# Kernel optimization log

Measured on AMD Instinct MI355X. Metric: run time of the kernel, lower is better.

Reference implementation:

```python
import jax, jax.numpy as jnp
import numpy as np

C = 256
D = C // 8  # query/key channels


def setup_inputs() -> dict:
    key = jax.random.key(0)
    ks = jax.random.split(key, 7)
    x = jax.random.normal(ks[0], (4, C, 64, 64), dtype=jnp.float32)
    s1 = 1.0 / np.sqrt(C)
    w1 = jax.random.normal(ks[1], (D, C), dtype=jnp.float32) * s1
    b1 = jax.random.normal(ks[2], (D,), dtype=jnp.float32) * 0.01
    w2 = jax.random.normal(ks[3], (D, C), dtype=jnp.float32) * s1
    b2 = jax.random.normal(ks[4], (D,), dtype=jnp.float32) * 0.01
    w3 = jax.random.normal(ks[5], (C, C), dtype=jnp.float32) * s1
    b3 = jax.random.normal(ks[6], (C,), dtype=jnp.float32) * 0.01
    return {"x": x, "w1": w1, "b1": b1, "w2": w2, "b2": b2, "w3": w3, "b3": b3}


def reference(x, w1, b1, w2, b2, w3, b3):
    B, Cc, W, H = x.shape
    N = W * H
    xf = x.reshape(B, Cc, N)  # [B, C, N] flattened spatial
    # 1x1 convs are per-pixel linear maps over channels
    q = jnp.einsum('dc,bcn->bnd', w1, xf) + b1  # [B, N, D]
    k = jnp.einsum('dc,bcn->bdn', w2, xf) + b2[:, None]  # [B, D, N]
    v = jnp.einsum('oc,bcn->bon', w3, xf) + b3[:, None]  # [B, C, N]
    energy = jnp.einsum('bnd,bdm->bnm', q, k)  # [B, N, N]
    attn = jax.nn.softmax(energy, axis=-1)
    out = jnp.einsum('bcm,bnm->bcn', v, attn)  # bmm(V, attn^T)
    out = out.reshape(B, Cc, W, H) + x
    return out
```

## Files before the change

kernel.cpp:

```cpp
#include <hip/hip_runtime.h>
#include <hip/hip_fp16.h>

typedef _Float16 half8 __attribute__((ext_vector_type(8)));
typedef _Float16 half2v __attribute__((ext_vector_type(2)));
typedef float f32x16 __attribute__((ext_vector_type(16)));
typedef float f32x4v __attribute__((ext_vector_type(4)));

#define MFMA16(A, B, C) __builtin_amdgcn_mfma_f32_32x32x16_f16((A), (B), (C), 0, 0, 0)

__device__ __forceinline__ f32x16 fzero16() {
  f32x16 z;
#pragma unroll
  for (int i = 0; i < 16; ++i) z[i] = 0.0f;
  return z;
}

__device__ __forceinline__ float max16(float vm, const f32x16& s) {
  const float g1 = fmaxf(fmaxf(s[0], s[1]), s[2]);
  const float g2 = fmaxf(fmaxf(s[3], s[4]), s[5]);
  const float g3 = fmaxf(fmaxf(s[6], s[7]), s[8]);
  const float g4 = fmaxf(fmaxf(s[9], s[10]), s[11]);
  const float g5 = fmaxf(fmaxf(s[12], s[13]), s[14]);
  const float h1 = fmaxf(fmaxf(g1, g2), g3);
  const float h2 = fmaxf(fmaxf(g4, g5), s[15]);
  return fmaxf(fmaxf(vm, h1), h2);
}

__global__ __launch_bounds__(256) void wprep_kernel(
    const float* __restrict__ w1, const float* __restrict__ w2,
    const float* __restrict__ w3,
    _Float16* __restrict__ w1p, _Float16* __restrict__ w2p,
    _Float16* __restrict__ w3p)
{
  const int t = threadIdx.x;
  const int blk = blockIdx.x;
  if (blk < 32) {
    const int cot = blk >> 2, sub = blk & 3;
    for (int e = sub * 2048 + t; e < sub * 2048 + 2048; e += 256) {
      const int j = e & 7, l = (e >> 3) & 63, cs = e >> 9;
      const int lr = l & 31, h = l >> 5;
      const int row = cot * 32 + lr;
      const int col = cs * 16 + 4 * h + (j & 3) + 8 * (j >> 2);
      w3p[((cot * 16 + cs) * 64 + l) * 8 + j] = (_Float16)w3[row * 256 + col];
    }
  } else {
    const int sub = blk - 32;
    for (int e = sub * 1024 + t; e < sub * 1024 + 1024; e += 256) {
      const int j = e & 7, l = (e >> 3) & 63, cs = e >> 9;
      const int lr = l & 31, h = l >> 5;
      const int col = cs * 16 + 4 * h + (j & 3) + 8 * (j >> 2);
      const int idx = (cs * 64 + l) * 8 + j;
      w1p[idx] = (_Float16)w1[lr * 256 + col];
      w2p[idx] = (_Float16)w2[lr * 256 + col];
    }
  }
}

__global__ __launch_bounds__(256) void qkv_proj_kernel(
    const float* __restrict__ x,
    const _Float16* __restrict__ w1p, const float* __restrict__ b1,
    const _Float16* __restrict__ w2p, const float* __restrict__ b2,
    const _Float16* __restrict__ w3p, const float* __restrict__ b3,
    _Float16* __restrict__ qb, _Float16* __restrict__ kb,
    _Float16* __restrict__ vb)
{
  __shared__ f32x4v red[4][2][4][64];
  const int t = threadIdx.x, w = t >> 6, l = t & 63;
  const int lr = l & 31, h = l >> 5;
  const int b = blockIdx.x >> 7;
  const int nt = blockIdx.x & 127;
  const float* xb = x + (size_t)b * 256 * 4096 + nt * 32 + lr;
  const int cot0 = w * 2, cot1 = w * 2 + 1;

  f32x16 accq = fzero16(), acck = fzero16();
  f32x16 accv0 = fzero16(), accv1 = fzero16();

  for (int cs = 0; cs < 16; ++cs) {
    const int c0 = cs * 16 + 4 * h;
    half8 xh;
#pragma unroll
    for (int j = 0; j < 8; ++j) {
      const int c = c0 + (j & 3) + 8 * (j >> 2);
      xh[j] = (_Float16)xb[(size_t)c * 4096];
    }
    const half8 wh0 = *(const half8*)&w3p[((cot0 * 16 + cs) * 64 + l) * 8];
    const half8 wh1 = *(const half8*)&w3p[((cot1 * 16 + cs) * 64 + l) * 8];
    accv0 = MFMA16(xh, wh0, accv0);
    accv1 = MFMA16(xh, wh1, accv1);
    if ((cs >> 2) == w) {
      const half8 w1h = *(const half8*)&w1p[(cs * 64 + l) * 8];
      const half8 w2h = *(const half8*)&w2p[(cs * 64 + l) * 8];
      accq = MFMA16(w1h, xh, accq);
      acck = MFMA16(w2h, xh, acck);
    }
  }

  const float bv0 = b3[cot0 * 32 + lr];
  const float bv1 = b3[cot1 * 32 + lr];
#pragma unroll
  for (int hfq = 0; hfq < 2; ++hfq) {
    half8 p0, p1;
#pragma unroll
    for (int j = 0; j < 8; ++j) {
      p0[j] = (_Float16)(accv0[8 * hfq + j] + bv0);
      p1[j] = (_Float16)(accv1[8 * hfq + j] + bv1);
    }
    const int ms = nt * 2 + hfq;
    *(half8*)&vb[((((size_t)b * 256 + ms) * 8 + cot0) * 64 + l) * 8] = p0;
    *(half8*)&vb[((((size_t)b * 256 + ms) * 8 + cot1) * 64 + l) * 8] = p1;
  }

#pragma unroll
  for (int i4 = 0; i4 < 4; ++i4) {
    f32x4v q4, k4;
#pragma unroll
    for (int c = 0; c < 4; ++c) { q4[c] = accq[4 * i4 + c]; k4[c] = acck[4 * i4 + c]; }
    red[w][0][i4][l] = q4;
    red[w][1][i4][l] = k4;
  }
  __syncthreads();
  if (w < 2) {
    _Float16* dst = (w == 0) ? qb : kb;
    const float* bias = (w == 0) ? b1 : b2;
    f32x16 tot;
#pragma unroll
    for (int i4 = 0; i4 < 4; ++i4) {
      f32x4v v = red[0][w][i4][l];
      v += red[1][w][i4][l];
      v += red[2][w][i4][l];
      v += red[3][w][i4][l];
#pragma unroll
      for (int c = 0; c < 4; ++c) tot[4 * i4 + c] = v[c];
    }
#pragma unroll
    for (int ds = 0; ds < 2; ++ds) {
      half8 ph;
#pragma unroll
      for (int j = 0; j < 8; ++j) {
        const int d = 16 * ds + 4 * h + (j & 3) + 8 * (j >> 2);
        ph[j] = (_Float16)(tot[8 * ds + j] + bias[d]);
      }
      *(half8*)&dst[((((size_t)b * 128 + nt) * 2 + ds) * 64 + l) * 8] = ph;
    }
  }
}

__global__ __launch_bounds__(512, 4) void attn_kernel(
    const _Float16* __restrict__ qb, const _Float16* __restrict__ kb,
    const _Float16* __restrict__ vb,
    const float* __restrict__ x, float* __restrict__ out)
{
  __shared__ __align__(16) _Float16 Plds[2][2][8][64][8];
  __shared__ float Lred[8][32];
  const int t = threadIdx.x, w = t >> 6, l = t & 63;
  const int lr = l & 31, h = l >> 5;
  const int bid = blockIdx.x;
  const int xcd = bid & 7;
  const int b = xcd >> 1;
  const int rg = ((bid >> 3) << 1) | (xcd & 1);
  const int ti = w >> 2;
  const int qq = w & 3;

  const _Float16* kbase = kb + (size_t)b * 131072 + (size_t)l * 8;
  const _Float16* vbase = vb + (size_t)b * 1048576 + (size_t)w * 512 + (size_t)l * 8;

#define KFM(m, ds) (*(const half8*)(kbase + ((size_t)((m) * 2 + (ds))) * 512))
#define VF(P, TI, ks) (*(const half8*)(vbase + ((size_t)(16 * (P) + 8 * (TI) + (ks))) * 4096))

  const _Float16* qp = qb + (((size_t)b * 128 + rg) * 2 * 64 + l) * 8;
  const half8 qf0 = *(const half8*)qp;
  const half8 qf1 = *(const half8*)(qp + 512);
  const float LOG2E = 1.44269504088896340736f;

  f32x16 acc = fzero16();
  float Lacc = 0.f;
  half8 va0[8], va1[8];
  half8 kc0, kc1;

#pragma unroll
  for (int ks = 0; ks < 8; ++ks) va0[ks] = VF(0, 0, ks);
#pragma unroll
  for (int ks = 0; ks < 8; ++ks) va1[ks] = VF(0, 1, ks);

  {
    float vm = -3.0e38f;
    half8 sk0 = KFM(16 * w, 0), sk1 = KFM(16 * w, 1);
    for (int m = 16 * w; m < 16 * w + 16; ++m) {
      half8 nk0, nk1;
      if (m + 1 < 16 * w + 16) { nk0 = KFM(m + 1, 0); nk1 = KFM(m + 1, 1); }
      f32x16 s = fzero16();
      s = MFMA16(sk0, qf0, s);
      s = MFMA16(sk1, qf1, s);
      vm = max16(vm, s);
      sk0 = nk0; sk1 = nk1;
    }
    vm = fmaxf(vm, __shfl_xor(vm, 32));
    if (l < 32) Lred[w][lr] = vm;
  }
  __syncthreads();
  float Mr = Lred[0][lr];
#pragma unroll
  for (int ww = 1; ww < 8; ++ww) Mr = fmaxf(Mr, Lred[ww][lr]);
  const float nM2 = -Mr * LOG2E;

#define EXPPACK(S, BUF)                                                        \
  {                                                                            \
    float pvv[16];                                                             \
    float ls = 0.f;                                                            \
    _Pragma("unroll") for (int i = 0; i < 16; ++i) {                           \
      pvv[i] = exp2f(fmaf((S)[i], LOG2E, nM2)); ls += pvv[i];                  \
    }                                                                          \
    Lacc += ls;                                                                \
    union { half8 v; half2v h2[4]; } u0, u1;                                   \
    _Pragma("unroll") for (int jj = 0; jj < 4; ++jj) {                         \
      auto a0 = __builtin_amdgcn_cvt_pkrtz(pvv[2 * jj], pvv[2 * jj + 1]);      \
      auto a1 = __builtin_amdgcn_cvt_pkrtz(pvv[8 + 2 * jj], pvv[8 + 2 * jj + 1]); \
      u0.h2[jj] = *(half2v*)&a0;                                               \
      u1.h2[jj] = *(half2v*)&a1;                                               \
    }                                                                          \
    *(half8*)&Plds[BUF][ti][qq * 2 + 0][l][0] = u0.v;                          \
    *(half8*)&Plds[BUF][ti][qq * 2 + 1][l][0] = u1.v;                          \
  }

#define PVC(CB, TI, VA)                                                        \
  {                                                                            \
    __builtin_amdgcn_s_setprio(1);                                             \
    _Pragma("unroll") for (int ks = 0; ks < 8; ++ks) {                         \
      const half8 pb = *(const half8*)&Plds[CB][TI][ks][l][0];                 \
      acc = MFMA16(VA[ks], pb, acc);                                           \
    }                                                                          \
    __builtin_amdgcn_s_setprio(0);                                             \
  }

  kc0 = KFM(w, 0); kc1 = KFM(w, 1);
  {
    f32x16 s = fzero16();
    s = MFMA16(kc0, qf0, s);
    s = MFMA16(kc1, qf1, s);
    kc0 = KFM(8 + w, 0); kc1 = KFM(8 + w, 1);
    EXPPACK(s, 0)
  }
  asm volatile("s_waitcnt lgkmcnt(0)" ::: "memory");
  __builtin_amdgcn_s_barrier();
  asm volatile("" ::: "memory");

  for (int P = 0; P < 16; ++P) {
    const int CB = P & 1, PB = CB ^ 1;

    if (P + 1 < 16) {
      f32x16 s = fzero16();
      s = MFMA16(kc0, qf0, s);
      s = MFMA16(kc1, qf1, s);
      if (P + 2 < 16) { kc0 = KFM(8 * (P + 2) + w, 0); kc1 = KFM(8 * (P + 2) + w, 1); }
      EXPPACK(s, PB)
    }
    PVC(CB, 0, va0)
    if (P + 1 < 16) {
#pragma unroll
      for (int ks = 0; ks < 8; ++ks) va0[ks] = VF(P + 1, 0, ks);
    }
    PVC(CB, 1, va1)
    if (P + 1 < 16) {
#pragma unroll
      for (int ks = 0; ks < 8; ++ks) va1[ks] = VF(P + 1, 1, ks);
    }

    asm volatile("s_waitcnt lgkmcnt(0)" ::: "memory");
    __builtin_amdgcn_s_barrier();
    asm volatile("" ::: "memory");
  }
#undef PVC
#undef EXPPACK
#undef KFM
#undef VF

  {
    const float l2 = Lacc + __shfl_xor(Lacc, 32);
    if (l < 32) Lred[w][lr] = l2;
  }
  __syncthreads();
  float Ls = Lred[0][lr];
#pragma unroll
  for (int ww = 1; ww < 8; ++ww) Ls += Lred[ww][lr];
  const float invL = 1.0f / Ls;

  const float* xb = x + (size_t)b * 1048576;
  float* ob = out + (size_t)b * 1048576;
  const int nn = rg * 32 + lr;
#pragma unroll
  for (int reg = 0; reg < 16; ++reg) {
    const int crel = (reg & 3) + 8 * (reg >> 2) + 4 * h;
    const int cout = w * 32 + crel;
    const size_t o = (size_t)cout * 4096 + nn;
    ob[o] = acc[reg] * invL + xb[o];
  }
}

extern "C" void kernel_launch(void* const* d_in, const int* in_sizes, int n_in,
                              void* d_out, int out_size, void* d_ws, size_t ws_size,
                              hipStream_t stream) {
  const float* x  = (const float*)d_in[0];
  const float* w1 = (const float*)d_in[1];
  const float* b1 = (const float*)d_in[2];
  const float* w2 = (const float*)d_in[3];
  const float* b2 = (const float*)d_in[4];
  const float* w3 = (const float*)d_in[5];
  const float* b3 = (const float*)d_in[6];
  float* out = (float*)d_out;

  char* ws = (char*)d_ws;
  _Float16* qb  = (_Float16*)(ws);
  _Float16* kb  = (_Float16*)(ws + (1u << 20));
  _Float16* vb  = (_Float16*)(ws + (2u << 20));
  _Float16* w1p = (_Float16*)(ws + (10u << 20) + (64u << 10));
  _Float16* w2p = (_Float16*)(ws + (10u << 20) + (96u << 10));
  _Float16* w3p = (_Float16*)(ws + (10u << 20) + (128u << 10));

  hipLaunchKernelGGL(wprep_kernel, dim3(40), dim3(256), 0, stream,
                     w1, w2, w3, w1p, w2p, w3p);
  hipLaunchKernelGGL(qkv_proj_kernel, dim3(512), dim3(256), 0, stream,
                     x, w1p, b1, w2p, b2, w3p, b3, qb, kb, vb);
  hipLaunchKernelGGL(attn_kernel, dim3(512), dim3(512), 0, stream,
                     qb, kb, vb, x, out);
}
```

Measured before the change: 82.96 us.

## Split attention over key ranges per wave with register-resident P and LDS reduction

The attention kernel now processes 64 query rows per block instead of 32, with each wave owning a quarter of the key range and consuming its softmax probabilities directly from registers as MFMA operands. This removes the LDS P buffer and the per-step block barriers. Partial output accumulators are instead combined across waves through a shared-memory reduction at the end. Output channels are handled in two passes, which recomputes QK^T and exp twice, and fewer blocks are launched with lower occupancy bounds, which raises register pressure.

```diff
diff --git a/kernel.cpp b/kernel.cpp
--- a/kernel.cpp
+++ b/kernel.cpp
@@ -145,49 +145,42 @@
   }
 }
 
-__global__ __launch_bounds__(512, 4) void attn_kernel(
+__global__ __launch_bounds__(512, 2) void attn_kernel(
     const _Float16* __restrict__ qb, const _Float16* __restrict__ kb,
     const _Float16* __restrict__ vb,
     const float* __restrict__ x, float* __restrict__ out)
 {
-  __shared__ __align__(16) _Float16 Plds[2][2][8][64][8];
-  __shared__ float Lred[8][32];
+  __shared__ float comb[8 * 2 * 16 * 64];
+  __shared__ float Mred[2][4][32];
+  __shared__ float Lred[2][4][32];
   const int t = threadIdx.x, w = t >> 6, l = t & 63;
   const int lr = l & 31, h = l >> 5;
   const int bid = blockIdx.x;
   const int xcd = bid & 7;
   const int b = xcd >> 1;
   const int rg = ((bid >> 3) << 1) | (xcd & 1);
-  const int ti = w >> 2;
-  const int qq = w & 3;
+  const int sw = w >> 2;
+  const int kq = w & 3;
+  const int m0 = kq * 32;
 
   const _Float16* kbase = kb + (size_t)b * 131072 + (size_t)l * 8;
-  const _Float16* vbase = vb + (size_t)b * 1048576 + (size_t)w * 512 + (size_t)l * 8;
+  const _Float16* vbase = vb + (size_t)b * 1048576 + (size_t)l * 8;
 
 #define KFM(m, ds) (*(const half8*)(kbase + ((size_t)((m) * 2 + (ds))) * 512))
-#define VF(P, TI, ks) (*(const half8*)(vbase + ((size_t)(16 * (P) + 8 * (TI) + (ks))) * 4096))
-
-  const _Float16* qp = qb + (((size_t)b * 128 + rg) * 2 * 64 + l) * 8;
+#define VFm(m, ks, ct, PS) (*(const half8*)(vbase + ((size_t)((((m) * 2 + (ks)) * 8) + ((PS) * 4 + (ct)))) * 512))
+
+  const int rt32q = rg * 2 + sw;
+  const _Float16* qp = qb + (((size_t)b * 128 + rt32q) * 2 * 64 + l) * 8;
   const half8 qf0 = *(const half8*)qp;
   const half8 qf1 = *(const half8*)(qp + 512);
   const float LOG2E = 1.44269504088896340736f;
 
-  f32x16 acc = fzero16();
-  float Lacc = 0.f;
-  half8 va0[8], va1[8];
-  half8 kc0, kc1;
-
-#pragma unroll
-  for (int ks = 0; ks < 8; ++ks) va0[ks] = VF(0, 0, ks);
-#pragma unroll
-  for (int ks = 0; ks < 8; ++ks) va1[ks] = VF(0, 1, ks);
-
   {
     float vm = -3.0e38f;
-    half8 sk0 = KFM(16 * w, 0), sk1 = KFM(16 * w, 1);
-    for (int m = 16 * w; m < 16 * w + 16; ++m) {
+    half8 sk0 = KFM(m0, 0), sk1 = KFM(m0, 1);
+    for (int m = m0; m < m0 + 32; ++m) {
       half8 nk0, nk1;
-      if (m + 1 < 16 * w + 16) { nk0 = KFM(m + 1, 0); nk1 = KFM(m + 1, 1); }
+      if (m + 1 < m0 + 32) { nk0 = KFM(m + 1, 0); nk1 = KFM(m + 1, 1); }
       f32x16 s = fzero16();
       s = MFMA16(sk0, qf0, s);
       s = MFMA16(sk1, qf1, s);
@@ -195,105 +188,118 @@
       sk0 = nk0; sk1 = nk1;
     }
     vm = fmaxf(vm, __shfl_xor(vm, 32));
-    if (l < 32) Lred[w][lr] = vm;
+    if (l < 32) Mred[sw][kq][lr] = vm;
   }
   __syncthreads();
-  float Mr = Lred[0][lr];
-#pragma unroll
-  for (int ww = 1; ww < 8; ++ww) Mr = fmaxf(Mr, Lred[ww][lr]);
+  const float Mr = fmaxf(fmaxf(Mred[sw][0][lr], Mred[sw][1][lr]),
+                         fmaxf(Mred[sw][2][lr], Mred[sw][3][lr]));
   const float nM2 = -Mr * LOG2E;
 
-#define EXPPACK(S, BUF)                                                        \
+  float Lacc = 0.f;
+  const float* xb = x + (size_t)b * 1048576;
+  float* ob = out + (size_t)b * 1048576;
+
+#define EXPP(S, PS)                                                            \
   {                                                                            \
     float pvv[16];                                                             \
     float ls = 0.f;                                                            \
     _Pragma("unroll") for (int i = 0; i < 16; ++i) {                           \
       pvv[i] = exp2f(fmaf((S)[i], LOG2E, nM2)); ls += pvv[i];                  \
     }                                                                          \
-    Lacc += ls;                                                                \
-    union { half8 v; half2v h2[4]; } u0, u1;                                   \
+    if ((PS) == 0) Lacc += ls;                                                 \
+    union { half8 v; half2v h2[4]; } uu0, uu1;                                 \
     _Pragma("unroll") for (int jj = 0; jj < 4; ++jj) {                         \
       auto a0 = __builtin_amdgcn_cvt_pkrtz(pvv[2 * jj], pvv[2 * jj + 1]);      \
       auto a1 = __builtin_amdgcn_cvt_pkrtz(pvv[8 + 2 * jj], pvv[8 + 2 * jj + 1]); \
-      u0.h2[jj] = *(half2v*)&a0;                                               \
-      u1.h2[jj] = *(half2v*)&a1;                                               \
+      uu0.h2[jj] = *(half2v*)&a0;                                              \
+      uu1.h2[jj] = *(half2v*)&a1;                                              \
     }                                                                          \
-    *(half8*)&Plds[BUF][ti][qq * 2 + 0][l][0] = u0.v;                          \
-    *(half8*)&Plds[BUF][ti][qq * 2 + 1][l][0] = u1.v;                          \
-  }
-
-#define PVC(CB, TI, VA)                                                        \
+    u0c = uu0.v; u1c = uu1.v;                                                  \
+  }
+
+#define PVCONS(VC)                                                             \
   {                                                                            \
     __builtin_amdgcn_s_setprio(1);                                             \
-    _Pragma("unroll") for (int ks = 0; ks < 8; ++ks) {                         \
-      const half8 pb = *(const half8*)&Plds[CB][TI][ks][l][0];                 \
-      acc = MFMA16(VA[ks], pb, acc);                                           \
+    _Pragma("unroll") for (int ct = 0; ct < 4; ++ct) {                         \
+      acc[ct] = MFMA16(VC[ct * 2 + 0], u0c, acc[ct]);                          \
+      acc[ct] = MFMA16(VC[ct * 2 + 1], u1c, acc[ct]);                          \
     }                                                                          \
     __builtin_amdgcn_s_setprio(0);                                             \
   }
 
-  kc0 = KFM(w, 0); kc1 = KFM(w, 1);
-  {
-    f32x16 s = fzero16();
-    s = MFMA16(kc0, qf0, s);
-    s = MFMA16(kc1, qf1, s);
-    kc0 = KFM(8 + w, 0); kc1 = KFM(8 + w, 1);
-    EXPPACK(s, 0)
-  }
-  asm volatile("s_waitcnt lgkmcnt(0)" ::: "memory");
-  __builtin_amdgcn_s_barrier();
-  asm volatile("" ::: "memory");
-
-  for (int P = 0; P < 16; ++P) {
-    const int CB = P & 1, PB = CB ^ 1;
-
-    if (P + 1 < 16) {
+#define PBODY(I, VC, VN, PS)                                                   \
+  {                                                                            \
+    _Pragma("unroll") for (int e = 0; e < 8; ++e)                              \
+      VN[e] = VFm(m0 + (I) + 1, (e)&1, (e) >> 1, PS);                          \
+    f32x16 s = fzero16();                                                      \
+    s = MFMA16(kc0, qf0, s);                                                   \
+    s = MFMA16(kc1, qf1, s);                                                   \
+    if ((I) + 2 < 32) { kc0 = KFM(m0 + (I) + 2, 0); kc1 = KFM(m0 + (I) + 2, 1); } \
+    PVCONS(VC)                                                                 \
+    EXPP(s, PS)                                                                \
+  }
+
+  for (int ps = 0; ps < 2; ++ps) {
+    f32x16 acc[4];
+#pragma unroll
+    for (int ct = 0; ct < 4; ++ct) acc[ct] = fzero16();
+    half8 VA[8], VB[8];
+    half8 kc0, kc1, u0c, u1c;
+
+#pragma unroll
+    for (int e = 0; e < 8; ++e) VA[e] = VFm(m0, e & 1, e >> 1, ps);
+    kc0 = KFM(m0, 0); kc1 = KFM(m0, 1);
+    {
       f32x16 s = fzero16();
       s = MFMA16(kc0, qf0, s);
       s = MFMA16(kc1, qf1, s);
-      if (P + 2 < 16) { kc0 = KFM(8 * (P + 2) + w, 0); kc1 = KFM(8 * (P + 2) + w, 1); }
-      EXPPACK(s, PB)
-    }
-    PVC(CB, 0, va0)
-    if (P + 1 < 16) {
-#pragma unroll
-      for (int ks = 0; ks < 8; ++ks) va0[ks] = VF(P + 1, 0, ks);
-    }
-    PVC(CB, 1, va1)
-    if (P + 1 < 16) {
-#pragma unroll
-      for (int ks = 0; ks < 8; ++ks) va1[ks] = VF(P + 1, 1, ks);
-    }
-
-    asm volatile("s_waitcnt lgkmcnt(0)" ::: "memory");
-    __builtin_amdgcn_s_barrier();
-    asm volatile("" ::: "memory");
-  }
-#undef PVC
-#undef EXPPACK
+      kc0 = KFM(m0 + 1, 0); kc1 = KFM(m0 + 1, 1);
+      EXPP(s, ps)
+    }
+
+    for (int i = 0; i < 30; i += 2) {
+      PBODY(i, VA, VB, ps)
+      PBODY(i + 1, VB, VA, ps)
+    }
+    PBODY(30, VA, VB, ps)
+    PVCONS(VB)
+
+    if (ps == 0) {
+      const float l2 = Lacc + __shfl_xor(Lacc, 32);
+      if (l < 32) Lred[sw][kq][lr] = l2;
+    }
+#pragma unroll
+    for (int c = 0; c < 2; ++c) {
+      __syncthreads();
+#pragma unroll
+      for (int ctc = 0; ctc < 2; ++ctc)
+#pragma unroll
+        for (int reg = 0; reg < 16; ++reg)
+          comb[((w * 2 + ctc) * 16 + reg) * 64 + l] = acc[c * 2 + ctc][reg];
+      __syncthreads();
+      const int s2 = w >> 2, ctc2 = (w >> 1) & 1, hf = w & 1;
+      const float invL = 1.0f / (Lred[s2][0][lr] + Lred[s2][1][lr] +
+                                 Lred[s2][2][lr] + Lred[s2][3][lr]);
+      const int nn = rg * 64 + s2 * 32 + lr;
+#pragma unroll
+      for (int r8 = 0; r8 < 8; ++r8) {
+        const int reg = hf * 8 + r8;
+        float sum = comb[(((s2 * 4 + 0) * 2 + ctc2) * 16 + reg) * 64 + l];
+        sum += comb[(((s2 * 4 + 1) * 2 + ctc2) * 16 + reg) * 64 + l];
+        sum += comb[(((s2 * 4 + 2) * 2 + ctc2) * 16 + reg) * 64 + l];
+        sum += comb[(((s2 * 4 + 3) * 2 + ctc2) * 16 + reg) * 64 + l];
+        const int crel = (reg & 3) + 8 * (reg >> 2) + 4 * h;
+        const int cout = (ps * 4 + c * 2 + ctc2) * 32 + crel;
+        const size_t o = (size_t)cout * 4096 + nn;
+        ob[o] = sum * invL + xb[o];
+      }
+    }
+  }
+#undef PBODY
+#undef PVCONS
+#undef EXPP
 #undef KFM
-#undef VF
-
-  {
-    const float l2 = Lacc + __shfl_xor(Lacc, 32);
-    if (l < 32) Lred[w][lr] = l2;
-  }
-  __syncthreads();
-  float Ls = Lred[0][lr];
-#pragma unroll
-  for (int ww = 1; ww < 8; ++ww) Ls += Lred[ww][lr];
-  const float invL = 1.0f / Ls;
-
-  const float* xb = x + (size_t)b * 1048576;
-  float* ob = out + (size_t)b * 1048576;
-  const int nn = rg * 32 + lr;
-#pragma unroll
-  for (int reg = 0; reg < 16; ++reg) {
-    const int crel = (reg & 3) + 8 * (reg >> 2) + 4 * h;
-    const int cout = w * 32 + crel;
-    const size_t o = (size_t)cout * 4096 + nn;
-    ob[o] = acc[reg] * invL + xb[o];
-  }
+#undef VFm
 }
 
 extern "C" void kernel_launch(void* const* d_in, const int* in_sizes, int n_in,
@@ -320,6 +326,6 @@
                      w1, w2, w3, w1p, w2p, w3p);
   hipLaunchKernelGGL(qkv_proj_kernel, dim3(512), dim3(256), 0, stream,
                      x, w1p, b1, w2p, b2, w3p, b3, qb, kb, vb);
-  hipLaunchKernelGGL(attn_kernel, dim3(512), dim3(512), 0, stream,
+  hipLaunchKernelGGL(attn_kernel, dim3(256), dim3(512), 0, stream,
                      qb, kb, vb, x, out);
 }
```

Result: slower. 99.13 us (+19.5%).
